# Kernel tuning notes

Measured on AMD Instinct MI355X. Metric: run time of the kernel, lower is better.

## Reference

```python
import jax, jax.numpy as jnp
import numpy as np

EPS = 1e-12  # F.normalize default eps


def setup_inputs() -> dict:
    key = jax.random.key(0)
    k1, k2 = jax.random.split(key)
    b, c, angRes, h, w = 4, 64, 5, 64, 64
    d = 64  # dims
    x = jax.random.normal(k1, (b, c, angRes * angRes, h, w), dtype=jnp.float32)
    # 1x1 conv weight [3*dims, channels] (kernel size 1, no bias)
    W = jax.random.normal(k2, (3 * d, c), dtype=jnp.float32) * 0.02
    return {"x": x, "W": W}


def reference(x, W):
    b, c, n, h, w = x.shape
    d = W.shape[0] // 3
    # 1x1 conv over angular (u,v) grid == channel matmul; rearranges are free reindexings
    qkv = jnp.einsum('oc,bcnhw->bonhw', W, x)  # [b, 3d, n, h, w]
    q, k, v = jnp.split(qkv, 3, axis=1)        # each [b, d, n, h, w]

    def flat(t):  # '(b h w) c u v -> b (u v) (c h w)'
        return t.transpose(0, 2, 1, 3, 4).reshape(b, n, d * h * w)

    q, k, v = flat(q), flat(k), flat(v)
    # L2-normalize along the (c h w) feature dim (k was normalized on dim=-2 of its
    # transposed layout, which is this same feature dim)
    q = q / jnp.maximum(jnp.linalg.norm(q, axis=-1, keepdims=True), EPS)
    k = k / jnp.maximum(jnp.linalg.norm(k, axis=-1, keepdims=True), EPS)
    att = jax.nn.softmax(jnp.einsum('bnf,bmf->bnm', q, k), axis=-1)  # [b, n, n], n=25
    out = jnp.einsum('bnm,bmf->bnf', att, v)   # [b, n, d*h*w]
    # 'b (u v) (c h w) -> b c (u v) h w'
    return out.reshape(b, n, d, h, w).transpose(0, 2, 1, 3, 4)
```

## Files before the change

kernel.cpp:

```cpp
#include <hip/hip_runtime.h>

#define B   4
#define C   64
#define D   64
#define NN  25
#define HW  4096
#define F   (D*HW)

#define SW  256
#define PT  128

typedef unsigned short ushort_t;
typedef unsigned int   uint_t;
typedef __attribute__((ext_vector_type(8)))  short  short8;
typedef __attribute__((ext_vector_type(16))) float  floatx16;
typedef __attribute__((ext_vector_type(4)))  float  f32x4;
typedef __attribute__((ext_vector_type(4)))  unsigned short us4;

__device__ ushort_t g_Wthi[128 * C];
__device__ ushort_t g_Wtlo[128 * C];
__device__ float    g_Wvt[C * 64];

static __device__ __forceinline__ ushort_t f2bf(float f) {
    uint_t u = __float_as_uint(f);
    u += 0x7FFFu + ((u >> 16) & 1u);
    return (ushort_t)(u >> 16);
}
static __device__ __forceinline__ float bf2f(ushort_t h) {
    return __uint_as_float((uint_t)h << 16);
}

static __device__ __forceinline__ int lds_x(int p, int c) {
    return p * 64 + ((((c >> 3) ^ (p & 7)) << 3) | (c & 7));
}

__global__ void k_zero(float* acc) {
    int i = blockIdx.x * 256 + threadIdx.x;
    if (i < 2700) acc[i] = 0.f;
}

__global__ void k_wprep(const float* __restrict__ W) {
    int i = blockIdx.x * 256 + threadIdx.x;
    if (i < 128 * 64) {
        float w = W[i];
        ushort_t hi = f2bf(w);
        g_Wthi[i] = hi;
        g_Wtlo[i] = f2bf(w - bf2f(hi));
    } else if (i < 192 * 64) {
        int j = i - 128 * 64;
        int d = j >> 6, c = j & 63;
        g_Wvt[c * 64 + d] = W[(128 + d) * 64 + c];
    }
}

__global__ void __launch_bounds__(256, 2)
k_qkmfma(const float* __restrict__ x,
         ushort_t* __restrict__ Q, ushort_t* __restrict__ K,
         float* __restrict__ qq, float* __restrict__ kk) {
    __shared__ ushort_t sXhi[PT * 64];
    __shared__ ushort_t sXlo[PT * 64];

    const int t  = threadIdx.x;
    const int wv = t >> 6, ln = t & 63;
    const int n  = blockIdx.y, b = blockIdx.z;
    const int gp0 = blockIdx.x * PT;

    {
        const int c16 = wv * 16;
#pragma unroll
        for (int cg = 0; cg < 4; ++cg) {
            const int c4 = c16 + cg * 4;
            const float* xc = x + ((size_t)(b * C + c4) * NN + n) * HW + gp0;
#pragma unroll
            for (int ph = 0; ph < 2; ++ph) {
                const int p = ph * 64 + ln;
                float v[4];
#pragma unroll
                for (int i = 0; i < 4; ++i) v[i] = xc[(size_t)i * NN * HW + p];
                us4 h, l;
#pragma unroll
                for (int i = 0; i < 4; ++i) {
                    ushort_t hi = f2bf(v[i]);
                    h[i] = hi;
                    l[i] = f2bf(v[i] - bf2f(hi));
                }
                *(us4*)&sXhi[lds_x(p, c4)] = h;
                *(us4*)&sXlo[lds_x(p, c4)] = l;
            }
        }
    }
    __syncthreads();

    const int row = ln & 31, kh = (ln >> 5) * 8, d0 = wv * 32;
    short8 ahi[4], alo[4];
#pragma unroll
    for (int ks = 0; ks < 4; ++ks) {
        ahi[ks] = *(const short8*)&g_Wthi[(d0 + row) * 64 + ks * 16 + kh];
        alo[ks] = *(const short8*)&g_Wtlo[(d0 + row) * 64 + ks * 16 + kh];
    }

    ushort_t* __restrict__ O = (wv < 2) ? Q : K;
    const int dbase = (wv < 2) ? d0 : (d0 - 64);
    const size_t obase = ((size_t)(b * NN + n) * D + dbase) * HW + gp0;

    float nrm = 0.f;
#pragma unroll
    for (int pt = 0; pt < 4; ++pt) {
        const int pcol = pt * 32 + (ln & 31);
        floatx16 acc;
#pragma unroll
        for (int r = 0; r < 16; ++r) acc[r] = 0.f;
#pragma unroll
        for (int ks = 0; ks < 4; ++ks) {
            const int c0 = ks * 16 + kh;
            short8 bhi = *(const short8*)&sXhi[lds_x(pcol, c0)];
            short8 blo = *(const short8*)&sXlo[lds_x(pcol, c0)];
            acc = __builtin_amdgcn_mfma_f32_32x32x16_bf16(ahi[ks], bhi, acc, 0, 0, 0);
            acc = __builtin_amdgcn_mfma_f32_32x32x16_bf16(alo[ks], bhi, acc, 0, 0, 0);
            acc = __builtin_amdgcn_mfma_f32_32x32x16_bf16(ahi[ks], blo, acc, 0, 0, 0);
        }
#pragma unroll
        for (int r = 0; r < 16; ++r) {
            const int dr = (r & 3) + 8 * (r >> 2) + 4 * (ln >> 5);
            nrm += acc[r] * acc[r];
            O[obase + (size_t)dr * HW + pcol] = f2bf(acc[r]);
        }
    }
    for (int off = 32; off > 0; off >>= 1) nrm += __shfl_xor(nrm, off);
    if (ln == 0) atomicAdd(((wv < 2) ? qq : kk) + b * NN + n, nrm);
}

__global__ void k_sqk(const ushort_t* __restrict__ Q, const ushort_t* __restrict__ K,
                      float* __restrict__ S) {
    const int t  = threadIdx.x;
    const int wv = t >> 6, ln = t & 63;
    const int b  = blockIdx.y;
    const int row  = ln & 31;
    const int rowc = (row < NN) ? row : (NN - 1);
    const int kh   = (ln >> 5) * 8;
    const size_t f0 = (size_t)blockIdx.x * (4 * SW) + (size_t)wv * SW;
    const ushort_t* Qp = Q + ((size_t)b * NN + rowc) * F + f0 + kh;
    const ushort_t* Kp = K + ((size_t)b * NN + rowc) * F + f0 + kh;

    floatx16 acc;
#pragma unroll
    for (int r = 0; r < 16; ++r) acc[r] = 0.f;

    for (int s = 0; s < SW / 16; ++s) {
        short8 aq = *(const short8*)(Qp + s * 16);
        short8 bk = *(const short8*)(Kp + s * 16);
        acc = __builtin_amdgcn_mfma_f32_32x32x16_bf16(aq, bk, acc, 0, 0, 0);
    }

    __shared__ float redS[4][64][17];
#pragma unroll
    for (int r = 0; r < 16; ++r) redS[wv][ln][r] = acc[r];
    __syncthreads();
    if (wv == 0) {
#pragma unroll
        for (int r = 0; r < 16; ++r) {
            float v = redS[0][ln][r] + redS[1][ln][r] + redS[2][ln][r] + redS[3][ln][r];
            const int srow = (r & 3) + 8 * (r >> 2) + 4 * (ln >> 5);
            const int scol = ln & 31;
            if (srow < NN && scol < NN)
                atomicAdd(&S[((size_t)b * NN + srow) * NN + scol], v);
        }
    }
}

__global__ void k_softmax(const float* __restrict__ S, const float* __restrict__ qq,
                          const float* __restrict__ kk, float* __restrict__ attT) {
    const int b = blockIdx.x, n = threadIdx.x;
    if (n >= NN) return;
    const float qn = fmaxf(sqrtf(qq[b * NN + n]), 1e-12f);
    float l[NN], mx = -1e30f;
#pragma unroll
    for (int m = 0; m < NN; ++m) {
        const float km = fmaxf(sqrtf(kk[b * NN + m]), 1e-12f);
        l[m] = S[((size_t)b * NN + n) * NN + m] / (qn * km);
        mx = fmaxf(mx, l[m]);
    }
    float s = 0.f;
#pragma unroll
    for (int m = 0; m < NN; ++m) { l[m] = expf(l[m] - mx); s += l[m]; }
    const float inv = 1.f / s;
#pragma unroll
    for (int m = 0; m < NN; ++m) attT[((size_t)b * NN + m) * NN + n] = l[m] * inv;
}

__global__ void k_mix(const float* __restrict__ x, const float* __restrict__ attT,
                      float* __restrict__ xa) {
    const int p = blockIdx.x * 256 + threadIdx.x;
    const int c = blockIdx.y, b = blockIdx.z;
    const float* xb = x + ((size_t)(b * C + c) * NN) * HW + p;
    const float* at = attT + (size_t)b * NN * NN;
    float acc[NN];
#pragma unroll
    for (int n = 0; n < NN; ++n) acc[n] = 0.f;
#pragma unroll 5
    for (int m = 0; m < NN; ++m) {
        const float xm = xb[(size_t)m * HW];
#pragma unroll
        for (int n = 0; n < NN; ++n) acc[n] += at[m * NN + n] * xm;
    }
#pragma unroll
    for (int n = 0; n < NN; ++n)
        xa[((size_t)(b * C + c) * NN + n) * HW + p] = acc[n];
}

__global__ void __launch_bounds__(256, 4)
k_vproj(const float* __restrict__ xa, float* __restrict__ out) {
    const int t   = threadIdx.x;
    const int wv  = __builtin_amdgcn_readfirstlane(t >> 6);
    const int ln  = t & 63;
    const int n   = blockIdx.y, b = blockIdx.z;
    const int p   = blockIdx.x * 256 + ln * 4;
    const int dp0 = wv * 16;

    const float* xb = xa + ((size_t)(b * C) * NN + n) * HW + p;

    float acc[16][4];
#pragma unroll
    for (int i = 0; i < 16; ++i)
#pragma unroll
        for (int j = 0; j < 4; ++j) acc[i][j] = 0.f;

#pragma unroll 4
    for (int c = 0; c < C; ++c) {
        const f32x4 xv = *(const f32x4*)(xb + (size_t)c * NN * HW);
        const float* wr = g_Wvt + c * 64 + dp0;
#pragma unroll
        for (int i = 0; i < 16; ++i) {
            const float w = wr[i];
#pragma unroll
            for (int j = 0; j < 4; ++j) acc[i][j] += w * xv[j];
        }
    }
#pragma unroll
    for (int i = 0; i < 16; ++i)
        *(f32x4*)(out + ((size_t)(b * D + dp0 + i) * NN + n) * HW + p) =
            *(const f32x4*)&acc[i][0];
}

extern "C" void kernel_launch(void* const* d_in, const int* in_sizes, int n_in,
                              void* d_out, int out_size, void* d_ws, size_t ws_size,
                              hipStream_t stream) {
    const float* x = (const float*)d_in[0];
    const float* W = (const float*)d_in[1];
    float* outf = (float*)d_out;

    ushort_t* Q  = (ushort_t*)d_ws;
    ushort_t* K  = Q + (size_t)B * NN * F;
    float*    xa = (float*)d_ws;

    float* S    = outf;
    float* qq   = outf + 2500;
    float* kk   = outf + 2600;
    float* attT = outf + 2700;

    k_zero   <<<dim3(11),             256, 0, stream>>>(outf);
    k_wprep  <<<dim3(48),             256, 0, stream>>>(W);
    k_qkmfma <<<dim3(HW/PT, NN, B),   256, 0, stream>>>(x, Q, K, qq, kk);
    k_sqk    <<<dim3(F/(4*SW), B),    256, 0, stream>>>(Q, K, S);
    k_softmax<<<dim3(B),               64, 0, stream>>>(S, qq, kk, attT);
    k_mix    <<<dim3(HW/256, C, B),   256, 0, stream>>>(x, attT, xa);
    k_vproj  <<<dim3(HW/256, NN, B),  256, 0, stream>>>(xa, outf);
}
```

Measured before the change: 343.5 us.

## Move V projection to split-bf16 MFMA, vectorize mix, halve QK pixel tile

The fp32 FMA V projection is replaced by an MFMA kernel that stages xa into LDS as hi/lo bf16 pairs and applies three bf16 products to approximate fp32 accuracy, matching the QK projection kernel. The QK projection tile shrinks from 128 to 64 pixels with a higher occupancy launch bound, and the LDS swizzle changes to suit the new layout. The mix kernel now processes four pixels per thread with vector loads and stores. Together these aim to cut ALU-bound time in the V projection and improve memory throughput, at the cost of small precision loss from the bf16 split and more blocks.

```diff
diff --git a/kernel.cpp b/kernel.cpp
--- a/kernel.cpp
+++ b/kernel.cpp
@@ -8,7 +8,7 @@
 #define F   (D*HW)
 
 #define SW  256
-#define PT  128
+#define PT  64
 
 typedef unsigned short ushort_t;
 typedef unsigned int   uint_t;
@@ -19,7 +19,8 @@
 
 __device__ ushort_t g_Wthi[128 * C];
 __device__ ushort_t g_Wtlo[128 * C];
-__device__ float    g_Wvt[C * 64];
+__device__ ushort_t g_Wvhi[D * C];
+__device__ ushort_t g_Wvlo[D * C];
 
 static __device__ __forceinline__ ushort_t f2bf(float f) {
     uint_t u = __float_as_uint(f);
@@ -31,7 +32,7 @@
 }
 
 static __device__ __forceinline__ int lds_x(int p, int c) {
-    return p * 64 + ((((c >> 3) ^ (p & 7)) << 3) | (c & 7));
+    return p * 64 + ((((c >> 3) ^ ((p >> 2) & 7)) << 3) | (c & 7));
 }
 
 __global__ void k_zero(float* acc) {
@@ -47,13 +48,15 @@
         g_Wthi[i] = hi;
         g_Wtlo[i] = f2bf(w - bf2f(hi));
     } else if (i < 192 * 64) {
+        float w = W[i];
         int j = i - 128 * 64;
-        int d = j >> 6, c = j & 63;
-        g_Wvt[c * 64 + d] = W[(128 + d) * 64 + c];
-    }
-}
-
-__global__ void __launch_bounds__(256, 2)
+        ushort_t hi = f2bf(w);
+        g_Wvhi[j] = hi;
+        g_Wvlo[j] = f2bf(w - bf2f(hi));
+    }
+}
+
+__global__ void __launch_bounds__(256, 8)
 k_qkmfma(const float* __restrict__ x,
          ushort_t* __restrict__ Q, ushort_t* __restrict__ K,
          float* __restrict__ qq, float* __restrict__ kk) {
@@ -71,22 +74,18 @@
         for (int cg = 0; cg < 4; ++cg) {
             const int c4 = c16 + cg * 4;
             const float* xc = x + ((size_t)(b * C + c4) * NN + n) * HW + gp0;
-#pragma unroll
-            for (int ph = 0; ph < 2; ++ph) {
-                const int p = ph * 64 + ln;
-                float v[4];
-#pragma unroll
-                for (int i = 0; i < 4; ++i) v[i] = xc[(size_t)i * NN * HW + p];
-                us4 h, l;
-#pragma unroll
-                for (int i = 0; i < 4; ++i) {
-                    ushort_t hi = f2bf(v[i]);
-                    h[i] = hi;
-                    l[i] = f2bf(v[i] - bf2f(hi));
-                }
-                *(us4*)&sXhi[lds_x(p, c4)] = h;
-                *(us4*)&sXlo[lds_x(p, c4)] = l;
+            float v[4];
+#pragma unroll
+            for (int i = 0; i < 4; ++i) v[i] = xc[(size_t)i * NN * HW + ln];
+            us4 h, l;
+#pragma unroll
+            for (int i = 0; i < 4; ++i) {
+                ushort_t hi = f2bf(v[i]);
+                h[i] = hi;
+                l[i] = f2bf(v[i] - bf2f(hi));
             }
+            *(us4*)&sXhi[lds_x(ln, c4)] = h;
+            *(us4*)&sXlo[lds_x(ln, c4)] = l;
         }
     }
     __syncthreads();
@@ -105,8 +104,8 @@
 
     float nrm = 0.f;
 #pragma unroll
-    for (int pt = 0; pt < 4; ++pt) {
-        const int pcol = pt * 32 + (ln & 31);
+    for (int pt = 0; pt < 2; ++pt) {
+        const int pcol = pt * 32 + row;
         floatx16 acc;
 #pragma unroll
         for (int r = 0; r < 16; ++r) acc[r] = 0.f;
@@ -188,58 +187,86 @@
     for (int m = 0; m < NN; ++m) attT[((size_t)b * NN + m) * NN + n] = l[m] * inv;
 }
 
-__global__ void k_mix(const float* __restrict__ x, const float* __restrict__ attT,
-                      float* __restrict__ xa) {
-    const int p = blockIdx.x * 256 + threadIdx.x;
+__global__ void __launch_bounds__(256, 4)
+k_mix(const float* __restrict__ x, const float* __restrict__ attT,
+      float* __restrict__ xa) {
+    const int p = (blockIdx.x * 256 + threadIdx.x) * 4;
     const int c = blockIdx.y, b = blockIdx.z;
     const float* xb = x + ((size_t)(b * C + c) * NN) * HW + p;
     const float* at = attT + (size_t)b * NN * NN;
-    float acc[NN];
+    f32x4 acc[NN];
 #pragma unroll
     for (int n = 0; n < NN; ++n) acc[n] = 0.f;
 #pragma unroll 5
     for (int m = 0; m < NN; ++m) {
-        const float xm = xb[(size_t)m * HW];
+        const f32x4 xm = *(const f32x4*)(xb + (size_t)m * HW);
 #pragma unroll
         for (int n = 0; n < NN; ++n) acc[n] += at[m * NN + n] * xm;
     }
 #pragma unroll
     for (int n = 0; n < NN; ++n)
-        xa[((size_t)(b * C + c) * NN + n) * HW + p] = acc[n];
-}
-
-__global__ void __launch_bounds__(256, 4)
+        *(f32x4*)&xa[((size_t)(b * C + c) * NN + n) * HW + p] = acc[n];
+}
+
+__global__ void __launch_bounds__(256, 8)
 k_vproj(const float* __restrict__ xa, float* __restrict__ out) {
-    const int t   = threadIdx.x;
-    const int wv  = __builtin_amdgcn_readfirstlane(t >> 6);
-    const int ln  = t & 63;
-    const int n   = blockIdx.y, b = blockIdx.z;
-    const int p   = blockIdx.x * 256 + ln * 4;
-    const int dp0 = wv * 16;
-
-    const float* xb = xa + ((size_t)(b * C) * NN + n) * HW + p;
-
-    float acc[16][4];
-#pragma unroll
-    for (int i = 0; i < 16; ++i)
-#pragma unroll
-        for (int j = 0; j < 4; ++j) acc[i][j] = 0.f;
-
-#pragma unroll 4
-    for (int c = 0; c < C; ++c) {
-        const f32x4 xv = *(const f32x4*)(xb + (size_t)c * NN * HW);
-        const float* wr = g_Wvt + c * 64 + dp0;
-#pragma unroll
-        for (int i = 0; i < 16; ++i) {
-            const float w = wr[i];
-#pragma unroll
-            for (int j = 0; j < 4; ++j) acc[i][j] += w * xv[j];
-        }
-    }
-#pragma unroll
-    for (int i = 0; i < 16; ++i)
-        *(f32x4*)(out + ((size_t)(b * D + dp0 + i) * NN + n) * HW + p) =
-            *(const f32x4*)&acc[i][0];
+    __shared__ ushort_t sXhi[PT * 64];
+    __shared__ ushort_t sXlo[PT * 64];
+
+    const int t  = threadIdx.x;
+    const int wv = t >> 6, ln = t & 63;
+    const int n  = blockIdx.y, b = blockIdx.z;
+    const int gp0 = blockIdx.x * PT;
+
+    {
+        const int c16 = wv * 16;
+#pragma unroll
+        for (int cg = 0; cg < 4; ++cg) {
+            const int c4 = c16 + cg * 4;
+            const float* xc = xa + ((size_t)(b * C + c4) * NN + n) * HW + gp0;
+            float v[4];
+#pragma unroll
+            for (int i = 0; i < 4; ++i) v[i] = xc[(size_t)i * NN * HW + ln];
+            us4 h, l;
+#pragma unroll
+            for (int i = 0; i < 4; ++i) {
+                ushort_t hi = f2bf(v[i]);
+                h[i] = hi;
+                l[i] = f2bf(v[i] - bf2f(hi));
+            }
+            *(us4*)&sXhi[lds_x(ln, c4)] = h;
+            *(us4*)&sXlo[lds_x(ln, c4)] = l;
+        }
+    }
+    __syncthreads();
+
+    const int row = ln & 31, kh = (ln >> 5) * 8;
+    const int d0  = (wv & 1) * 32;
+    short8 ahi[4], alo[4];
+#pragma unroll
+    for (int ks = 0; ks < 4; ++ks) {
+        ahi[ks] = *(const short8*)&g_Wvhi[(d0 + row) * 64 + ks * 16 + kh];
+        alo[ks] = *(const short8*)&g_Wvlo[(d0 + row) * 64 + ks * 16 + kh];
+    }
+
+    const int pcol = (wv >> 1) * 32 + row;
+    floatx16 acc;
+#pragma unroll
+    for (int r = 0; r < 16; ++r) acc[r] = 0.f;
+#pragma unroll
+    for (int ks = 0; ks < 4; ++ks) {
+        const int c0 = ks * 16 + kh;
+        short8 bhi = *(const short8*)&sXhi[lds_x(pcol, c0)];
+        short8 blo = *(const short8*)&sXlo[lds_x(pcol, c0)];
+        acc = __builtin_amdgcn_mfma_f32_32x32x16_bf16(ahi[ks], bhi, acc, 0, 0, 0);
+        acc = __builtin_amdgcn_mfma_f32_32x32x16_bf16(alo[ks], bhi, acc, 0, 0, 0);
+        acc = __builtin_amdgcn_mfma_f32_32x32x16_bf16(ahi[ks], blo, acc, 0, 0, 0);
+    }
+#pragma unroll
+    for (int r = 0; r < 16; ++r) {
+        const int dr = (r & 3) + 8 * (r >> 2) + 4 * (ln >> 5);
+        out[((size_t)(b * D + d0 + dr) * NN + n) * HW + gp0 + pcol] = acc[r];
+    }
 }
 
 extern "C" void kernel_launch(void* const* d_in, const int* in_sizes, int n_in,
@@ -263,6 +290,6 @@
     k_qkmfma <<<dim3(HW/PT, NN, B),   256, 0, stream>>>(x, Q, K, qq, kk);
     k_sqk    <<<dim3(F/(4*SW), B),    256, 0, stream>>>(Q, K, S);
     k_softmax<<<dim3(B),               64, 0, stream>>>(S, qq, kk, attT);
-    k_mix    <<<dim3(HW/256, C, B),   256, 0, stream>>>(x, attT, xa);
-    k_vproj  <<<dim3(HW/256, NN, B),  256, 0, stream>>>(xa, outf);
-}
+    k_mix    <<<dim3(HW/1024, C, B),  256, 0, stream>>>(x, attT, xa);
+    k_vproj  <<<dim3(HW/PT, NN, B),   256, 0, stream>>>(xa, outf);
+}
```

After: 367.0 us. 6.8% more time.
